# Optimization experiments

Measured on AMD Instinct MI355X. Metric: run time of the kernel, lower is better.

## Reference

```python
import jax, jax.numpy as jnp
import numpy as np
import math

N_NODES = 100000
N_EDGES = 1600000
D_FEAT = 32
K = 1        # Bernstein index k
N_ORD = 2    # Bernstein order n
COMB = float(math.comb(N_ORD, K))


def setup_inputs() -> dict:
    key = jax.random.key(0)
    k1, k2, k3 = jax.random.split(key, 3)
    feat = jax.random.normal(k1, (N_NODES, D_FEAT), dtype=jnp.float32)
    edge_src = jax.random.randint(k2, (N_EDGES,), 0, N_NODES)
    edge_dst = jax.random.randint(k3, (N_EDGES,), 0, N_NODES)
    return {"feat": feat, "edge_src": edge_src, "edge_dst": edge_dst}


def reference(feat, edge_src, edge_dst):
    # in-degree of each node (copy_u/sum aggregates over incoming edges)
    deg = jax.ops.segment_sum(jnp.ones((N_EDGES,), feat.dtype), edge_dst,
                              num_segments=N_NODES)
    d_invsqrt = jnp.clip(deg, 1.0, None) ** -0.5  # [N]
    d_invsqrt = d_invsqrt[:, None]                 # [N,1]

    def unn_laplacian(x):
        msg = (x * d_invsqrt)[edge_src]            # [E,D]
        agg = jax.ops.segment_sum(msg, edge_dst, num_segments=N_NODES)
        return x - agg * d_invsqrt

    if K == 0:
        h = feat
        for _ in range(N_ORD):
            h = unn_laplacian(h) / 2
            h = feat - h
    elif K == N_ORD:
        h = feat
        for _ in range(N_ORD):
            h = unn_laplacian(h) / 2
    else:
        temp = feat
        for _ in range(K):
            temp = unn_laplacian(temp) / 2
        h = feat
        for _ in range(N_ORD - K):
            h = unn_laplacian(h) / 2
            h = feat - h
        h = temp * h
    return COMB * h
```

## Files before the change

### kernel.cpp

```cpp
#include <hip/hip_runtime.h>

#define N_NODES 100000
#define N_EDGES 1600000
#define D_FEAT 32

#define BSH 8
#define BMASK 255
#define NB 391
#define CAPB 4864

#define P1_BS 512
#define P1_TILE 4096
#define P1_CAP 32


__global__ void init_kernel(int* __restrict__ cursorA) {
    int b = blockIdx.x * blockDim.x + threadIdx.x;
    if (b < NB) cursorA[b] = b * CAPB;
}

__global__ void __launch_bounds__(P1_BS)
bucket_kernel(const int* __restrict__ edge_src,
              const int* __restrict__ edge_dst,
              int* __restrict__ cursorA,
              int* __restrict__ pairs, int n_edges) {
    __shared__ int s_cnt[NB];
    __shared__ int s_base[NB];
    __shared__ int s_off[NB + 1];
    __shared__ int s_buf[NB * P1_CAP];

    int tile = blockIdx.x * P1_TILE;
    if (tile >= n_edges) return;

    for (int b = threadIdx.x; b < NB; b += P1_BS) s_cnt[b] = 0;
    __syncthreads();

    const int4* src4 = reinterpret_cast<const int4*>(edge_src);
    const int4* dst4 = reinterpret_cast<const int4*>(edge_dst);
    int tileq = blockIdx.x * (P1_TILE / 4);
    #pragma unroll
    for (int j = 0; j < P1_TILE / 4 / P1_BS; ++j) {
        int iq = tileq + j * P1_BS + threadIdx.x;
        if (iq * 4 < n_edges) {
            int4 sv = src4[iq];
            int4 dv = dst4[iq];
            int ss[4] = {sv.x, sv.y, sv.z, sv.w};
            int dd[4] = {dv.x, dv.y, dv.z, dv.w};
            #pragma unroll
            for (int u = 0; u < 4; ++u) {
                int b = dd[u] >> BSH;
                int packed = (ss[u] << BSH) | (dd[u] & BMASK);
                int p = atomicAdd(&s_cnt[b], 1);
                if (p < P1_CAP) {
                    s_buf[b * P1_CAP + p] = packed;
                } else {
                    int gp = atomicAdd(&cursorA[b], 1);
                    pairs[gp] = packed;
                }
            }
        }
    }
    __syncthreads();

    for (int b = threadIdx.x; b < NB; b += P1_BS) {
        int c = min(s_cnt[b], P1_CAP);
        s_base[b] = atomicAdd(&cursorA[b], c);
        s_cnt[b] = c;
    }
    __syncthreads();
    if (threadIdx.x == 0) {
        int acc = 0;
        for (int b = 0; b < NB; ++b) { s_off[b] = acc; acc += s_cnt[b]; }
        s_off[NB] = acc;
    }
    __syncthreads();

    int total = s_off[NB];
    for (int t = threadIdx.x; t < total; t += P1_BS) {
        int lo = 0, hi = NB;
        while (hi - lo > 1) {
            int mid = (lo + hi) >> 1;
            if (t >= s_off[mid]) lo = mid; else hi = mid;
        }
        int idx = t - s_off[lo];
        pairs[s_base[lo] + idx] = s_buf[lo * P1_CAP + idx];
    }
}

__global__ void __launch_bounds__(256)
sort_kernel(const int* __restrict__ pairs,
            const int* __restrict__ cursorA,
            int* __restrict__ ssrc,
            int* __restrict__ start,
            int* __restrict__ endv,
            float* __restrict__ dinv) {
    __shared__ int buf[CAPB];
    __shared__ int outb[CAPB];
    __shared__ int h[256];
    __shared__ int sc[256];
    __shared__ int cur[256];

    int b = blockIdx.x;
    int t = threadIdx.x;
    int base = b * CAPB;
    int cnt = min(cursorA[b] - base, CAPB);

    h[t] = 0;
    __syncthreads();
    for (int i = t; i < cnt; i += 256) {
        int p = pairs[base + i];
        buf[i] = p;
        atomicAdd(&h[p & BMASK], 1);
    }
    __syncthreads();

    int v = h[t];
    sc[t] = v;
    __syncthreads();
    for (int off = 1; off < 256; off <<= 1) {
        int x = (t >= off) ? sc[t - off] : 0;
        __syncthreads();
        sc[t] += x;
        __syncthreads();
    }
    int ex = sc[t] - v;
    cur[t] = ex;
    int node = (b << BSH) + t;
    if (node < N_NODES) {
        start[node] = base + ex;
        endv[node] = base + ex + v;
        dinv[node] = rsqrtf(fmaxf((float)v, 1.0f));
    }
    __syncthreads();

    for (int i = t; i < cnt; i += 256) {
        int p = buf[i];
        int pos = atomicAdd(&cur[p & BMASK], 1);
        outb[pos] = p >> BSH;
    }
    __syncthreads();
    for (int i = t; i < cnt; i += 256)
        ssrc[base + i] = outb[i];
}

__global__ void sf_kernel(const float* __restrict__ feat,
                          const float* __restrict__ dinv,
                          float* __restrict__ sfeat) {
    int gid = blockIdx.x * blockDim.x + threadIdx.x;
    int total = N_NODES * 8;
    if (gid < total) {
        float dv = dinv[gid >> 3];
        float4 fv = reinterpret_cast<const float4*>(feat)[gid];
        fv.x *= dv; fv.y *= dv; fv.z *= dv; fv.w *= dv;
        reinterpret_cast<float4*>(sfeat)[gid] = fv;
    }
}

__global__ void gather_sf_kernel(const float* __restrict__ feat,
                                 const float* __restrict__ sfeat,
                                 const int* __restrict__ start,
                                 const int* __restrict__ endv,
                                 const int* __restrict__ ssrc,
                                 const float* __restrict__ dinv,
                                 float* __restrict__ out) {
    int gid = blockIdx.x * blockDim.x + threadIdx.x;
    int node = gid >> 3;
    int fq = gid & 7;
    if (node >= N_NODES) return;
    int k = start[node];
    int en = endv[node];
    const float4* sf4 = reinterpret_cast<const float4*>(sfeat);
    float4 acc = make_float4(0.f, 0.f, 0.f, 0.f);
    for (; k + 3 < en; k += 4) {
        int s0 = ssrc[k],     s1 = ssrc[k + 1];
        int s2 = ssrc[k + 2], s3 = ssrc[k + 3];
        float4 f0 = sf4[s0 * 8 + fq];
        float4 f1 = sf4[s1 * 8 + fq];
        float4 f2 = sf4[s2 * 8 + fq];
        float4 f3 = sf4[s3 * 8 + fq];
        acc.x += f0.x + f1.x + f2.x + f3.x;
        acc.y += f0.y + f1.y + f2.y + f3.y;
        acc.z += f0.z + f1.z + f2.z + f3.z;
        acc.w += f0.w + f1.w + f2.w + f3.w;
    }
    for (; k < en; ++k) {
        int s = ssrc[k];
        float4 fv = sf4[s * 8 + fq];
        acc.x += fv.x; acc.y += fv.y; acc.z += fv.z; acc.w += fv.w;
    }
    float dvn = dinv[node];
    float4 fv = reinterpret_cast<const float4*>(feat)[node * 8 + fq];
    float4 o;
    float yx = 0.5f * (fv.x - acc.x * dvn);
    float yy = 0.5f * (fv.y - acc.y * dvn);
    float yz = 0.5f * (fv.z - acc.z * dvn);
    float yw = 0.5f * (fv.w - acc.w * dvn);
    o.x = 2.0f * yx * (fv.x - yx);
    o.y = 2.0f * yy * (fv.y - yy);
    o.z = 2.0f * yz * (fv.z - yz);
    o.w = 2.0f * yw * (fv.w - yw);
    reinterpret_cast<float4*>(out)[gid] = o;
}

__global__ void gather_kernel(const float* __restrict__ feat,
                              const int* __restrict__ start,
                              const int* __restrict__ endv,
                              const int* __restrict__ ssrc,
                              const float* __restrict__ dinv,
                              float* __restrict__ out) {
    int gid = blockIdx.x * blockDim.x + threadIdx.x;
    int node = gid >> 3;
    int fq = gid & 7;
    if (node >= N_NODES) return;
    int k = start[node];
    int en = endv[node];
    const float4* feat4 = reinterpret_cast<const float4*>(feat);
    float4 acc = make_float4(0.f, 0.f, 0.f, 0.f);
    for (; k < en; ++k) {
        int s = ssrc[k];
        float dv = dinv[s];
        float4 fv = feat4[s * 8 + fq];
        acc.x += fv.x * dv; acc.y += fv.y * dv;
        acc.z += fv.z * dv; acc.w += fv.w * dv;
    }
    float dvn = dinv[node];
    float4 fv = feat4[node * 8 + fq];
    float4 o;
    float yx = 0.5f * (fv.x - acc.x * dvn);
    float yy = 0.5f * (fv.y - acc.y * dvn);
    float yz = 0.5f * (fv.z - acc.z * dvn);
    float yw = 0.5f * (fv.w - acc.w * dvn);
    o.x = 2.0f * yx * (fv.x - yx);
    o.y = 2.0f * yy * (fv.y - yy);
    o.z = 2.0f * yz * (fv.z - yz);
    o.w = 2.0f * yw * (fv.w - yw);
    reinterpret_cast<float4*>(out)[gid] = o;
}

extern "C" void kernel_launch(void* const* d_in, const int* in_sizes, int n_in,
                              void* d_out, int out_size, void* d_ws, size_t ws_size,
                              hipStream_t stream) {
    const float* feat = (const float*)d_in[0];
    const int* edge_src = (const int*)d_in[1];
    const int* edge_dst = (const int*)d_in[2];
    float* out = (float*)d_out;

    int* ws = (int*)d_ws;
    int* cursorA = ws;
    int* start   = cursorA + 512;
    int* endv    = start + N_NODES;
    float* dinv  = (float*)(endv + N_NODES);
    int* ssrc    = (int*)(dinv + N_NODES);
    int* pairs   = ssrc + NB * CAPB;
    float* sfeat = (float*)pairs;

    size_t need_sf = ((size_t)(512 + 3 * N_NODES + NB * CAPB) +
                      (size_t)N_NODES * D_FEAT) * 4;
    bool use_sf = ws_size >= need_sf;

    init_kernel<<<1, 512, 0, stream>>>(cursorA);
    {
        int blocks = (N_EDGES + P1_TILE - 1) / P1_TILE;
        bucket_kernel<<<blocks, P1_BS, 0, stream>>>(edge_src, edge_dst,
                                                    cursorA, pairs, N_EDGES);
    }
    sort_kernel<<<NB, 256, 0, stream>>>(pairs, cursorA, ssrc, start, endv, dinv);
    int total = N_NODES * 8;
    int blocks = (total + 255) / 256;
    if (use_sf) {
        sf_kernel<<<blocks, 256, 0, stream>>>(feat, dinv, sfeat);
        gather_sf_kernel<<<blocks, 256, 0, stream>>>(feat, sfeat, start, endv,
                                                     ssrc, dinv, out);
    } else {
        gather_kernel<<<blocks, 256, 0, stream>>>(feat, start, endv,
                                                  ssrc, dinv, out);
    }
}
```

Before: 140.2 us.

## Halve bucket width, fuse feature prescale into sort kernel, pack node ranges

Buckets now cover 128 nodes instead of 256, doubling the bucket count to 782 and halving per-bucket capacity and per-tile staging capacity. The separate prescale kernel is removed: each sort block writes dinv-scaled features for its own nodes, using degree values kept in shared memory. Start and end offsets are packed into one int2, so the gather kernel does a single load per node. This saves a launch and an extra dinv read pass, but half the threads sit idle during the scan, and the smaller P1_CAP may overflow more often in the bucketing stage. The non-workspace fallback path is dropped.

```diff
diff --git a/kernel.cpp b/kernel.cpp
--- a/kernel.cpp
+++ b/kernel.cpp
@@ -4,14 +4,14 @@
 #define N_EDGES 1600000
 #define D_FEAT 32
 
-#define BSH 8
-#define BMASK 255
-#define NB 391
-#define CAPB 4864
+#define BSH 7
+#define BMASK 127
+#define NB 782
+#define CAPB 2432
 
 #define P1_BS 512
 #define P1_TILE 4096
-#define P1_CAP 32
+#define P1_CAP 16
 
 
 __global__ void init_kernel(int* __restrict__ cursorA) {
@@ -90,22 +90,24 @@
 __global__ void __launch_bounds__(256)
 sort_kernel(const int* __restrict__ pairs,
             const int* __restrict__ cursorA,
+            const float* __restrict__ feat,
             int* __restrict__ ssrc,
-            int* __restrict__ start,
-            int* __restrict__ endv,
-            float* __restrict__ dinv) {
+            int2* __restrict__ srange,
+            float* __restrict__ dinv,
+            float* __restrict__ sfeat) {
     __shared__ int buf[CAPB];
     __shared__ int outb[CAPB];
-    __shared__ int h[256];
-    __shared__ int sc[256];
-    __shared__ int cur[256];
+    __shared__ int h[128];
+    __shared__ int sc[128];
+    __shared__ int cur[128];
+    __shared__ float dv_s[128];
 
     int b = blockIdx.x;
     int t = threadIdx.x;
     int base = b * CAPB;
     int cnt = min(cursorA[b] - base, CAPB);
 
-    h[t] = 0;
+    if (t < 128) h[t] = 0;
     __syncthreads();
     for (int i = t; i < cnt; i += 256) {
         int p = pairs[base + i];
@@ -114,22 +116,26 @@
     }
     __syncthreads();
 
-    int v = h[t];
-    sc[t] = v;
-    __syncthreads();
-    for (int off = 1; off < 256; off <<= 1) {
-        int x = (t >= off) ? sc[t - off] : 0;
+    int v = 0;
+    if (t < 128) { v = h[t]; sc[t] = v; }
+    __syncthreads();
+    for (int off = 1; off < 128; off <<= 1) {
+        int x = 0;
+        if (t < 128 && t >= off) x = sc[t - off];
         __syncthreads();
-        sc[t] += x;
+        if (t < 128) sc[t] += x;
         __syncthreads();
     }
-    int ex = sc[t] - v;
-    cur[t] = ex;
-    int node = (b << BSH) + t;
-    if (node < N_NODES) {
-        start[node] = base + ex;
-        endv[node] = base + ex + v;
-        dinv[node] = rsqrtf(fmaxf((float)v, 1.0f));
+    if (t < 128) {
+        int ex = sc[t] - v;
+        cur[t] = ex;
+        int node = (b << BSH) + t;
+        if (node < N_NODES) {
+            srange[node] = make_int2(base + ex, base + ex + v);
+            float dvv = rsqrtf(fmaxf((float)v, 1.0f));
+            dinv[node] = dvv;
+            dv_s[t] = dvv;
+        }
     }
     __syncthreads();
 
@@ -141,25 +147,23 @@
     __syncthreads();
     for (int i = t; i < cnt; i += 256)
         ssrc[base + i] = outb[i];
-}
-
-__global__ void sf_kernel(const float* __restrict__ feat,
-                          const float* __restrict__ dinv,
-                          float* __restrict__ sfeat) {
-    int gid = blockIdx.x * blockDim.x + threadIdx.x;
-    int total = N_NODES * 8;
-    if (gid < total) {
-        float dv = dinv[gid >> 3];
-        float4 fv = reinterpret_cast<const float4*>(feat)[gid];
-        fv.x *= dv; fv.y *= dv; fv.z *= dv; fv.w *= dv;
-        reinterpret_cast<float4*>(sfeat)[gid] = fv;
+
+    const float4* feat4 = reinterpret_cast<const float4*>(feat);
+    float4* sf4 = reinterpret_cast<float4*>(sfeat);
+    for (int idx = t; idx < 128 * 8; idx += 256) {
+        int nl = idx >> 3;
+        int node = (b << BSH) + nl;
+        if (node >= N_NODES) continue;
+        float dvv = dv_s[nl];
+        float4 fv = feat4[node * 8 + (idx & 7)];
+        fv.x *= dvv; fv.y *= dvv; fv.z *= dvv; fv.w *= dvv;
+        sf4[node * 8 + (idx & 7)] = fv;
     }
 }
 
 __global__ void gather_sf_kernel(const float* __restrict__ feat,
                                  const float* __restrict__ sfeat,
-                                 const int* __restrict__ start,
-                                 const int* __restrict__ endv,
+                                 const int2* __restrict__ srange,
                                  const int* __restrict__ ssrc,
                                  const float* __restrict__ dinv,
                                  float* __restrict__ out) {
@@ -167,8 +171,8 @@
     int node = gid >> 3;
     int fq = gid & 7;
     if (node >= N_NODES) return;
-    int k = start[node];
-    int en = endv[node];
+    int2 se = srange[node];
+    int k = se.x, en = se.y;
     const float4* sf4 = reinterpret_cast<const float4*>(sfeat);
     float4 acc = make_float4(0.f, 0.f, 0.f, 0.f);
     for (; k + 3 < en; k += 4) {
@@ -202,41 +206,6 @@
     reinterpret_cast<float4*>(out)[gid] = o;
 }
 
-__global__ void gather_kernel(const float* __restrict__ feat,
-                              const int* __restrict__ start,
-                              const int* __restrict__ endv,
-                              const int* __restrict__ ssrc,
-                              const float* __restrict__ dinv,
-                              float* __restrict__ out) {
-    int gid = blockIdx.x * blockDim.x + threadIdx.x;
-    int node = gid >> 3;
-    int fq = gid & 7;
-    if (node >= N_NODES) return;
-    int k = start[node];
-    int en = endv[node];
-    const float4* feat4 = reinterpret_cast<const float4*>(feat);
-    float4 acc = make_float4(0.f, 0.f, 0.f, 0.f);
-    for (; k < en; ++k) {
-        int s = ssrc[k];
-        float dv = dinv[s];
-        float4 fv = feat4[s * 8 + fq];
-        acc.x += fv.x * dv; acc.y += fv.y * dv;
-        acc.z += fv.z * dv; acc.w += fv.w * dv;
-    }
-    float dvn = dinv[node];
-    float4 fv = feat4[node * 8 + fq];
-    float4 o;
-    float yx = 0.5f * (fv.x - acc.x * dvn);
-    float yy = 0.5f * (fv.y - acc.y * dvn);
-    float yz = 0.5f * (fv.z - acc.z * dvn);
-    float yw = 0.5f * (fv.w - acc.w * dvn);
-    o.x = 2.0f * yx * (fv.x - yx);
-    o.y = 2.0f * yy * (fv.y - yy);
-    o.z = 2.0f * yz * (fv.z - yz);
-    o.w = 2.0f * yw * (fv.w - yw);
-    reinterpret_cast<float4*>(out)[gid] = o;
-}
-
 extern "C" void kernel_launch(void* const* d_in, const int* in_sizes, int n_in,
                               void* d_out, int out_size, void* d_ws, size_t ws_size,
                               hipStream_t stream) {
@@ -246,33 +215,25 @@
     float* out = (float*)d_out;
 
     int* ws = (int*)d_ws;
-    int* cursorA = ws;
-    int* start   = cursorA + 512;
-    int* endv    = start + N_NODES;
-    float* dinv  = (float*)(endv + N_NODES);
-    int* ssrc    = (int*)(dinv + N_NODES);
-    int* pairs   = ssrc + NB * CAPB;
-    float* sfeat = (float*)pairs;
-
-    size_t need_sf = ((size_t)(512 + 3 * N_NODES + NB * CAPB) +
-                      (size_t)N_NODES * D_FEAT) * 4;
-    bool use_sf = ws_size >= need_sf;
-
-    init_kernel<<<1, 512, 0, stream>>>(cursorA);
+    int* cursorA  = ws;
+    int2* srange  = (int2*)(cursorA + 1024);
+    float* dinv   = (float*)(srange + N_NODES);
+    int* ssrc     = (int*)(dinv + N_NODES);
+    int* pairs    = ssrc + NB * CAPB;
+    float* sfeat  = (float*)(pairs + NB * CAPB);
+
+    init_kernel<<<1, 1024, 0, stream>>>(cursorA);
     {
         int blocks = (N_EDGES + P1_TILE - 1) / P1_TILE;
         bucket_kernel<<<blocks, P1_BS, 0, stream>>>(edge_src, edge_dst,
                                                     cursorA, pairs, N_EDGES);
     }
-    sort_kernel<<<NB, 256, 0, stream>>>(pairs, cursorA, ssrc, start, endv, dinv);
-    int total = N_NODES * 8;
-    int blocks = (total + 255) / 256;
-    if (use_sf) {
-        sf_kernel<<<blocks, 256, 0, stream>>>(feat, dinv, sfeat);
-        gather_sf_kernel<<<blocks, 256, 0, stream>>>(feat, sfeat, start, endv,
+    sort_kernel<<<NB, 256, 0, stream>>>(pairs, cursorA, feat, ssrc, srange,
+                                        dinv, sfeat);
+    {
+        int total = N_NODES * 8;
+        int blocks = (total + 255) / 256;
+        gather_sf_kernel<<<blocks, 256, 0, stream>>>(feat, sfeat, srange,
                                                      ssrc, dinv, out);
-    } else {
-        gather_kernel<<<blocks, 256, 0, stream>>>(feat, start, endv,
-                                                  ssrc, dinv, out);
-    }
-}
+    }
+}
```

New measurement: 142.3 us. About the same (+1.5%).
